# Optimization experiments

Measured on AMD Instinct MI355X. Metric: run time of the kernel, lower is better.

Reference implementation:

```python
import jax, jax.numpy as jnp
import numpy as np


def setup_inputs() -> dict:
    key = jax.random.key(0)
    k1, k2, k3 = jax.random.split(key, 3)
    B, C, H, W = 64, 2048, 14, 14
    M, NC = 32, 396
    x = jax.random.normal(k1, (B, C, H, W), dtype=jnp.float32)
    Wa = jax.random.normal(k2, (M, C), dtype=jnp.float32) * (1.0 / np.sqrt(C))
    ba = jnp.zeros((M,), dtype=jnp.float32)
    Wc = jax.random.normal(k3, (NC, M * C), dtype=jnp.float32) * (1.0 / np.sqrt(M * C))
    bc = jnp.zeros((NC,), dtype=jnp.float32)
    return {"x": x, "Wa": Wa, "ba": ba, "Wc": Wc, "bc": bc}


def reference(x, Wa, ba, Wc, bc):
    # x: [B, C, H, W]
    B, C, H, W = x.shape
    M = Wa.shape[0]
    # 1x1 conv == channel contraction; attention maps [B, M, H, W]
    A = jax.nn.sigmoid(jnp.einsum('bchw,mc->bmhw', x, Wa) + ba[None, :, None, None])
    # BAP: per-head attention-weighted global average pool -> [B, M, C]
    bap = jnp.einsum('bchw,bmhw->bmc', x, A) / (H * W)
    feats = bap.reshape(B, M * C)  # concat head-major, matching torch cat order
    return feats @ Wc.T + bc
```

## Files before the change

kernel.cpp:

```cpp
#include <hip/hip_runtime.h>
#include <hip/hip_bf16.h>
#include <cstdint>

#define B_N 64
#define C_N 2048
#define HW_N 196
#define HWP 224
#define M_N 32
#define NC_N 396
#define K_N 65536
#define CCH 256
#define NCH 8
#define KCH 64
#define ZSTRIDE (B_N * M_N * HW_N)

typedef __attribute__((ext_vector_type(8))) short bf16x8;
typedef __attribute__((ext_vector_type(4))) float f32x4;

__device__ inline short f2bf(float x) {
  union { float f; unsigned u; } v; v.f = x;
  unsigned r = (v.u + 0x7FFFu + ((v.u >> 16) & 1u)) >> 16;
  return (short)r;
}

__device__ inline unsigned packbf2(float lo, float hi) {
  return ((unsigned)(unsigned short)f2bf(hi) << 16) |
         (unsigned)(unsigned short)f2bf(lo);
}

__global__ __launch_bounds__(256) void k1a_partial(
    const float* __restrict__ x, const float* __restrict__ Wa,
    float* __restrict__ z) {
  __shared__ short waT[32][264];
  __shared__ short xT[2][208][40];
  const int t = threadIdx.x;
  const int w = t >> 6, lane = t & 63, lq = lane >> 4, ln = lane & 15;
  const int cx = blockIdx.x, b = blockIdx.y;
  const int c0 = cx * CCH;

  unsigned* xTw0 = (unsigned*)xT[0];
  unsigned* xTw1 = (unsigned*)xT[1];
  if (t < 240) { xTw0[196 * 20 + t] = 0u; xTw1[196 * 20 + t] = 0u; }
  for (int i = t; i < 2048; i += 256) {
    int m = i >> 6, f4 = i & 63;
    float4 v = *(const float4*)(Wa + (size_t)m * C_N + c0 + f4 * 4);
    uint2 pk;
    pk.x = packbf2(v.x, v.y);
    pk.y = packbf2(v.z, v.w);
    *(uint2*)((char*)waT + m * 528 + f4 * 8) = pk;
  }

  f32x4 acc[4][2];
#pragma unroll
  for (int ti = 0; ti < 4; ++ti) {
    acc[ti][0] = (f32x4){0.f, 0.f, 0.f, 0.f};
    acc[ti][1] = (f32x4){0.f, 0.f, 0.f, 0.f};
  }

  const float* __restrict__ xb0 = x + (size_t)b * (C_N * HW_N) + (size_t)c0 * HW_N;
  const int p0 = t & 15;
  const int q0 = t >> 4;

  float4 fa0, fb0, fa1, fb1, fa2, fb2, fa3, fb3;
  auto LD = [&](int ss) {
    const float* xs = xb0 + (size_t)ss * 32 * HW_N;
    const float* r0 = xs + (2 * p0) * HW_N + 4 * q0;
    fa0 = *(const float4*)r0;
    fb0 = *(const float4*)(r0 + HW_N);
    fa1 = *(const float4*)(r0 + 64);
    fb1 = *(const float4*)(r0 + 64 + HW_N);
    fa2 = *(const float4*)(r0 + 128);
    fb2 = *(const float4*)(r0 + 128 + HW_N);
    if (t < 16) {
      const float* r3 = xs + (2 * t) * HW_N + 192;
      fa3 = *(const float4*)r3;
      fb3 = *(const float4*)(r3 + HW_N);
    }
  };
  auto STORE = [&](unsigned* xw) {
    unsigned* d0 = xw + q0 * 80 + p0;
    d0[0]  = packbf2(fa0.x, fb0.x);
    d0[20] = packbf2(fa0.y, fb0.y);
    d0[40] = packbf2(fa0.z, fb0.z);
    d0[60] = packbf2(fa0.w, fb0.w);
    unsigned* d1 = d0 + 1280;
    d1[0]  = packbf2(fa1.x, fb1.x);
    d1[20] = packbf2(fa1.y, fb1.y);
    d1[40] = packbf2(fa1.z, fb1.z);
    d1[60] = packbf2(fa1.w, fb1.w);
    unsigned* d2 = d0 + 2560;
    d2[0]  = packbf2(fa2.x, fb2.x);
    d2[20] = packbf2(fa2.y, fb2.y);
    d2[40] = packbf2(fa2.z, fb2.z);
    d2[60] = packbf2(fa2.w, fb2.w);
    if (t < 16) {
      unsigned* d3 = xw + 48 * 80 + t;
      d3[0]  = packbf2(fa3.x, fb3.x);
      d3[20] = packbf2(fa3.y, fb3.y);
      d3[40] = packbf2(fa3.z, fb3.z);
      d3[60] = packbf2(fa3.w, fb3.w);
    }
  };

  LD(0);
  STORE(xTw0);
  __syncthreads();

  for (int ss = 0; ss < 8; ++ss) {
    if (ss < 7) LD(ss + 1);
    const char* xb = (const char*)xT[ss & 1];
    const int kb = ss * 64 + lq * 16;
    bf16x8 af0 = *(const bf16x8*)((const char*)waT + ln * 528 + kb);
    bf16x8 af1 = *(const bf16x8*)((const char*)waT + (16 + ln) * 528 + kb);
#pragma unroll
    for (int ti = 0; ti < 4; ++ti) {
      int ht = w + ti * 4;
      if (ht < 13) {
        bf16x8 bfr = *(const bf16x8*)(xb + (ht * 16 + ln) * 80 + lq * 16);
        acc[ti][0] = __builtin_amdgcn_mfma_f32_16x16x32_bf16(af0, bfr, acc[ti][0], 0, 0, 0);
        acc[ti][1] = __builtin_amdgcn_mfma_f32_16x16x32_bf16(af1, bfr, acc[ti][1], 0, 0, 0);
      }
    }
    if (ss < 7) STORE((ss & 1) ? xTw0 : xTw1);
    __syncthreads();
  }

  float* zc = z + (size_t)(cx * B_N + b) * (M_N * HW_N);
#pragma unroll
  for (int ti = 0; ti < 4; ++ti) {
    int ht = w + ti * 4;
    if (ht < 13) {
      int hw = ht * 16 + ln;
      if (hw < HW_N) {
#pragma unroll
        for (int mt = 0; mt < 2; ++mt) {
#pragma unroll
          for (int r = 0; r < 4; ++r) {
            int m = mt * 16 + lq * 4 + r;
            zc[(size_t)m * HW_N + hw] = acc[ti][mt][r];
          }
        }
      }
    }
  }
}

__global__ __launch_bounds__(256) void k1b_sig(
    const float* __restrict__ z, const float* __restrict__ ba,
    short* __restrict__ Apad) {
  int idx = blockIdx.x * 256 + threadIdx.x;
  int b = idx / (M_N * HWP);
  int r = idx - b * (M_N * HWP);
  int m = r / HWP;
  int hw = r - m * HWP;
  short out = 0;
  if (hw < HW_N) {
    float s = ba[m];
    size_t base = ((size_t)b * M_N + m) * HW_N + hw;
#pragma unroll
    for (int cx = 0; cx < NCH; ++cx)
      s += z[(size_t)cx * ZSTRIDE + base];
    out = f2bf(1.f / (1.f + __expf(-s)));
  }
  Apad[idx] = out;
}

__global__ __launch_bounds__(256) void k2_bap(
    const float* __restrict__ x, const short* __restrict__ Apad,
    short* __restrict__ featsb) {
  __shared__ short tb[8192];
  const int t = threadIdx.x;
  const int w = t >> 6, lane = t & 63, lq = lane >> 4, ln = lane & 15;
  const int cx = blockIdx.x;
  const int bq = blockIdx.y;
  const int cl = w * 16 + ln;
  const int c = cx * 64 + cl;
  const float sc = 1.f / (float)HW_N;
  const int och = cl >> 5, lq2w = (cl >> 3) & 3, j = cl & 7;

#pragma unroll
  for (int bi = 0; bi < 4; ++bi) {
    const int b = bq * 4 + bi;
    const float* __restrict__ xrow = x + (size_t)b * (C_N * HW_N) + (size_t)c * HW_N;
    const short* __restrict__ ap0 = Apad + ((size_t)b * M_N + ln) * HWP + lq * 8;
    const short* __restrict__ ap1 = ap0 + 16 * HWP;

    f32x4 d0 = {0.f, 0.f, 0.f, 0.f}, d1 = {0.f, 0.f, 0.f, 0.f};
#pragma unroll
    for (int s = 0; s < 7; ++s) {
      bf16x8 a0 = *(const bf16x8*)(ap0 + s * 32);
      bf16x8 a1 = *(const bf16x8*)(ap1 + s * 32);
      bf16x8 bfr;
      const int h = s * 32 + lq * 8;
      if (s < 6) {
        float4 b0 = *(const float4*)(xrow + h);
        float4 b1 = *(const float4*)(xrow + h + 4);
        bfr[0]=f2bf(b0.x); bfr[1]=f2bf(b0.y); bfr[2]=f2bf(b0.z); bfr[3]=f2bf(b0.w);
        bfr[4]=f2bf(b1.x); bfr[5]=f2bf(b1.y); bfr[6]=f2bf(b1.z); bfr[7]=f2bf(b1.w);
      } else {
        float4 b0 = make_float4(0.f, 0.f, 0.f, 0.f);
        if (lq == 0) b0 = *(const float4*)(xrow + h);
        bfr[0]=f2bf(b0.x); bfr[1]=f2bf(b0.y); bfr[2]=f2bf(b0.z); bfr[3]=f2bf(b0.w);
        bfr[4]=0; bfr[5]=0; bfr[6]=0; bfr[7]=0;
      }
      d0 = __builtin_amdgcn_mfma_f32_16x16x32_bf16(a0, bfr, d0, 0, 0, 0);
      d1 = __builtin_amdgcn_mfma_f32_16x16x32_bf16(a1, bfr, d1, 0, 0, 0);
    }
#pragma unroll
    for (int r = 0; r < 4; ++r) {
      int m0 = lq * 4 + r;
      tb[m0 * 256 + och * 128 + lq2w * 32 + bi * 8 + j]        = f2bf(d0[r] * sc);
      tb[(16 + m0) * 256 + och * 128 + lq2w * 32 + bi * 8 + j] = f2bf(d1[r] * sc);
    }
  }
  __syncthreads();

  const int me = t >> 3, oche = (t >> 2) & 1, lq2e = t & 3;
  const short* srcp = tb + t * 32;
  uint4 v0 = *(const uint4*)(srcp);
  uint4 v1 = *(const uint4*)(srcp + 8);
  uint4 v2 = *(const uint4*)(srcp + 16);
  uint4 v3 = *(const uint4*)(srcp + 24);
  const int sg = me * 64 + cx * 2 + oche;
  const int bt = bq >> 2;
  short* dst = featsb + (size_t)(sg * 4 + bt) * 512 + lq2e * 128 + (bq & 3) * 32;
  *(uint4*)(dst)      = v0;
  *(uint4*)(dst + 8)  = v1;
  *(uint4*)(dst + 16) = v2;
  *(uint4*)(dst + 24) = v3;
}

__global__ __launch_bounds__(256) void k3_cls(
    const short* __restrict__ featsb, const float* __restrict__ Wc,
    float* __restrict__ partial) {
  const int t = threadIdx.x;
  const int w = t >> 6, lane = t & 63, lq = lane >> 4, ln = lane & 15;
  const int n = blockIdx.x * 64 + w * 16 + ln;
  const int nc = n < NC_N ? n : NC_N - 1;
  const int kc = blockIdx.y;
  const size_t k0 = (size_t)kc * 1024;
  const float* __restrict__ wrow = Wc + (size_t)nc * K_N + k0 + lq * 8;
  const short* __restrict__ fb = featsb + (size_t)(kc * 32) * 2048 + lane * 8;

  f32x4 acc0 = {0.f,0.f,0.f,0.f}, acc1 = {0.f,0.f,0.f,0.f};
  f32x4 acc2 = {0.f,0.f,0.f,0.f}, acc3 = {0.f,0.f,0.f,0.f};

  float4 cw0 = *(const float4*)(wrow);
  float4 cw1 = *(const float4*)(wrow + 4);
  bf16x8 ca0 = *(const bf16x8*)(fb);
  bf16x8 ca1 = *(const bf16x8*)(fb + 512);
  bf16x8 ca2 = *(const bf16x8*)(fb + 1024);
  bf16x8 ca3 = *(const bf16x8*)(fb + 1536);

#pragma unroll
  for (int s = 0; s < 32; ++s) {
    float4 nw0, nw1; bf16x8 na0, na1, na2, na3;
    if (s < 31) {
      const float* wn = wrow + (s + 1) * 32;
      nw0 = *(const float4*)(wn);
      nw1 = *(const float4*)(wn + 4);
      const short* fs = fb + (size_t)(s + 1) * 2048;
      na0 = *(const bf16x8*)(fs);
      na1 = *(const bf16x8*)(fs + 512);
      na2 = *(const bf16x8*)(fs + 1024);
      na3 = *(const bf16x8*)(fs + 1536);
    }
    bf16x8 bfr;
    bfr[0]=f2bf(cw0.x); bfr[1]=f2bf(cw0.y); bfr[2]=f2bf(cw0.z); bfr[3]=f2bf(cw0.w);
    bfr[4]=f2bf(cw1.x); bfr[5]=f2bf(cw1.y); bfr[6]=f2bf(cw1.z); bfr[7]=f2bf(cw1.w);
    acc0 = __builtin_amdgcn_mfma_f32_16x16x32_bf16(ca0, bfr, acc0, 0, 0, 0);
    acc1 = __builtin_amdgcn_mfma_f32_16x16x32_bf16(ca1, bfr, acc1, 0, 0, 0);
    acc2 = __builtin_amdgcn_mfma_f32_16x16x32_bf16(ca2, bfr, acc2, 0, 0, 0);
    acc3 = __builtin_amdgcn_mfma_f32_16x16x32_bf16(ca3, bfr, acc3, 0, 0, 0);
    if (s < 31) {
      cw0 = nw0; cw1 = nw1;
      ca0 = na0; ca1 = na1; ca2 = na2; ca3 = na3;
    }
  }
  if (n < NC_N) {
    float* po = partial + (size_t)kc * (B_N * NC_N) + n;
#pragma unroll
    for (int r = 0; r < 4; ++r) {
      int br = lq * 4 + r;
      po[(size_t)br * NC_N]        = acc0[r];
      po[(size_t)(16 + br) * NC_N] = acc1[r];
      po[(size_t)(32 + br) * NC_N] = acc2[r];
      po[(size_t)(48 + br) * NC_N] = acc3[r];
    }
  }
}

__global__ __launch_bounds__(256) void k4_reduce(
    const float* __restrict__ partial, const float* __restrict__ bc,
    float* __restrict__ out) {
  int idx = blockIdx.x * 256 + threadIdx.x;
  if (idx >= B_N * NC_N) return;
  int n = idx % NC_N;
  float s = bc[n];
#pragma unroll 8
  for (int kc = 0; kc < KCH; ++kc) s += partial[(size_t)kc * (B_N * NC_N) + idx];
  out[idx] = s;
}

extern "C" void kernel_launch(void* const* d_in, const int* in_sizes, int n_in,
                              void* d_out, int out_size, void* d_ws, size_t ws_size,
                              hipStream_t stream) {
  const float* x  = (const float*)d_in[0];
  const float* Wa = (const float*)d_in[1];
  const float* ba = (const float*)d_in[2];
  const float* Wc = (const float*)d_in[3];
  const float* bc = (const float*)d_in[4];
  float* out = (float*)d_out;

  char* wsb = (char*)d_ws;
  short* Apad    = (short*)(wsb);
  short* featsb  = (short*)(wsb + (1u  << 20));
  float* partial = (float*)(wsb + (10u << 20));
  float* zbuf    = (float*)(wsb + (10u << 20));
  (void)ws_size; (void)in_sizes; (void)n_in; (void)out_size;

  hipLaunchKernelGGL(k1a_partial, dim3(NCH, B_N), dim3(256), 0, stream,
                     x, Wa, zbuf);
  hipLaunchKernelGGL(k1b_sig, dim3(1792), dim3(256), 0, stream,
                     zbuf, ba, Apad);
  hipLaunchKernelGGL(k2_bap, dim3(32, 16), dim3(256), 0, stream,
                     x, Apad, featsb);
  hipLaunchKernelGGL(k3_cls, dim3(7, KCH), dim3(256), 0, stream,
                     featsb, Wc, partial);
  hipLaunchKernelGGL(k4_reduce, dim3(99), dim3(256), 0, stream,
                     partial, bc, out);
}
```

Before: 270.5 us.

## Halve channel/K chunks, batch-interleave BAP loads, triple-buffer classifier prefetch

Halves the per-block channel chunk in the attention-logit kernel, which doubles the grid, and halves the K chunk in the classifier, which doubles the split-K partials. Padding rows of the x tile are now masked in registers instead of zero-filled in shared memory. The BAP kernel interleaves its four batches inside each step and prefetches the next step's x loads across all of them. The classifier moves to a three-slot register prefetch pipeline. More blocks and deeper prefetch aim to raise occupancy and hide memory latency, at the cost of more partial-sum traffic, a longer reduction, and more register pressure.

```diff
diff --git a/kernel.cpp b/kernel.cpp
--- a/kernel.cpp
+++ b/kernel.cpp
@@ -9,9 +9,9 @@
 #define M_N 32
 #define NC_N 396
 #define K_N 65536
-#define CCH 256
-#define NCH 8
-#define KCH 64
+#define CCH 128
+#define NCH 16
+#define KCH 128
 #define ZSTRIDE (B_N * M_N * HW_N)
 
 typedef __attribute__((ext_vector_type(8))) short bf16x8;
@@ -31,8 +31,8 @@
 __global__ __launch_bounds__(256) void k1a_partial(
     const float* __restrict__ x, const float* __restrict__ Wa,
     float* __restrict__ z) {
-  __shared__ short waT[32][264];
-  __shared__ short xT[2][208][40];
+  __shared__ short waT[32][136];
+  __shared__ short xT[2][196][40];
   const int t = threadIdx.x;
   const int w = t >> 6, lane = t & 63, lq = lane >> 4, ln = lane & 15;
   const int cx = blockIdx.x, b = blockIdx.y;
@@ -40,14 +40,13 @@
 
   unsigned* xTw0 = (unsigned*)xT[0];
   unsigned* xTw1 = (unsigned*)xT[1];
-  if (t < 240) { xTw0[196 * 20 + t] = 0u; xTw1[196 * 20 + t] = 0u; }
-  for (int i = t; i < 2048; i += 256) {
-    int m = i >> 6, f4 = i & 63;
+  for (int i = t; i < 1024; i += 256) {
+    int m = i >> 5, f4 = i & 31;
     float4 v = *(const float4*)(Wa + (size_t)m * C_N + c0 + f4 * 4);
     uint2 pk;
     pk.x = packbf2(v.x, v.y);
     pk.y = packbf2(v.z, v.w);
-    *(uint2*)((char*)waT + m * 528 + f4 * 8) = pk;
+    *(uint2*)((char*)waT + m * 272 + f4 * 8) = pk;
   }
 
   f32x4 acc[4][2];
@@ -106,22 +105,26 @@
   STORE(xTw0);
   __syncthreads();
 
-  for (int ss = 0; ss < 8; ++ss) {
-    if (ss < 7) LD(ss + 1);
+  const bf16x8 bzero = {0, 0, 0, 0, 0, 0, 0, 0};
+  for (int ss = 0; ss < 4; ++ss) {
+    if (ss < 3) LD(ss + 1);
     const char* xb = (const char*)xT[ss & 1];
     const int kb = ss * 64 + lq * 16;
-    bf16x8 af0 = *(const bf16x8*)((const char*)waT + ln * 528 + kb);
-    bf16x8 af1 = *(const bf16x8*)((const char*)waT + (16 + ln) * 528 + kb);
+    bf16x8 af0 = *(const bf16x8*)((const char*)waT + ln * 272 + kb);
+    bf16x8 af1 = *(const bf16x8*)((const char*)waT + (16 + ln) * 272 + kb);
 #pragma unroll
     for (int ti = 0; ti < 4; ++ti) {
       int ht = w + ti * 4;
       if (ht < 13) {
-        bf16x8 bfr = *(const bf16x8*)(xb + (ht * 16 + ln) * 80 + lq * 16);
+        int hwrow = ht * 16 + ln;
+        int rr = hwrow < HW_N ? hwrow : 0;
+        bf16x8 v = *(const bf16x8*)(xb + rr * 80 + lq * 16);
+        bf16x8 bfr = (hwrow < HW_N) ? v : bzero;
         acc[ti][0] = __builtin_amdgcn_mfma_f32_16x16x32_bf16(af0, bfr, acc[ti][0], 0, 0, 0);
         acc[ti][1] = __builtin_amdgcn_mfma_f32_16x16x32_bf16(af1, bfr, acc[ti][1], 0, 0, 0);
       }
     }
-    if (ss < 7) STORE((ss & 1) ? xTw0 : xTw1);
+    if (ss < 3) STORE((ss & 1) ? xTw0 : xTw1);
     __syncthreads();
   }
 
@@ -177,40 +180,73 @@
   const int c = cx * 64 + cl;
   const float sc = 1.f / (float)HW_N;
   const int och = cl >> 5, lq2w = (cl >> 3) & 3, j = cl & 7;
-
+  const size_t bstr = (size_t)C_N * HW_N;
+  const float* __restrict__ xrow0 = x + (size_t)(bq * 4) * bstr + (size_t)c * HW_N;
+
+  const short* apb[4];
+#pragma unroll
+  for (int bi = 0; bi < 4; ++bi)
+    apb[bi] = Apad + ((size_t)(bq * 4 + bi) * M_N + ln) * HWP + lq * 8;
+
+  f32x4 d0[4], d1[4];
 #pragma unroll
   for (int bi = 0; bi < 4; ++bi) {
-    const int b = bq * 4 + bi;
-    const float* __restrict__ xrow = x + (size_t)b * (C_N * HW_N) + (size_t)c * HW_N;
-    const short* __restrict__ ap0 = Apad + ((size_t)b * M_N + ln) * HWP + lq * 8;
-    const short* __restrict__ ap1 = ap0 + 16 * HWP;
-
-    f32x4 d0 = {0.f, 0.f, 0.f, 0.f}, d1 = {0.f, 0.f, 0.f, 0.f};
-#pragma unroll
-    for (int s = 0; s < 7; ++s) {
-      bf16x8 a0 = *(const bf16x8*)(ap0 + s * 32);
-      bf16x8 a1 = *(const bf16x8*)(ap1 + s * 32);
+    d0[bi] = (f32x4){0.f, 0.f, 0.f, 0.f};
+    d1[bi] = (f32x4){0.f, 0.f, 0.f, 0.f};
+  }
+
+  float4 xa[4], xc[4];
+#pragma unroll
+  for (int bi = 0; bi < 4; ++bi) {
+    const float* p = xrow0 + bi * bstr + lq * 8;
+    xa[bi] = *(const float4*)p;
+    xc[bi] = *(const float4*)(p + 4);
+  }
+
+#pragma unroll
+  for (int s = 0; s < 7; ++s) {
+    float4 na[4], nc[4];
+    if (s < 6) {
+      if (s + 1 < 6) {
+        const int h = (s + 1) * 32 + lq * 8;
+#pragma unroll
+        for (int bi = 0; bi < 4; ++bi) {
+          const float* p = xrow0 + bi * bstr + h;
+          na[bi] = *(const float4*)p;
+          nc[bi] = *(const float4*)(p + 4);
+        }
+      } else {
+#pragma unroll
+        for (int bi = 0; bi < 4; ++bi) {
+          float4 z4 = make_float4(0.f, 0.f, 0.f, 0.f);
+          na[bi] = z4; nc[bi] = z4;
+          if (lq == 0) na[bi] = *(const float4*)(xrow0 + bi * bstr + 192);
+        }
+      }
+    }
+#pragma unroll
+    for (int bi = 0; bi < 4; ++bi) {
+      bf16x8 a0 = *(const bf16x8*)(apb[bi] + s * 32);
+      bf16x8 a1 = *(const bf16x8*)(apb[bi] + 16 * HWP + s * 32);
       bf16x8 bfr;
-      const int h = s * 32 + lq * 8;
-      if (s < 6) {
-        float4 b0 = *(const float4*)(xrow + h);
-        float4 b1 = *(const float4*)(xrow + h + 4);
-        bfr[0]=f2bf(b0.x); bfr[1]=f2bf(b0.y); bfr[2]=f2bf(b0.z); bfr[3]=f2bf(b0.w);
-        bfr[4]=f2bf(b1.x); bfr[5]=f2bf(b1.y); bfr[6]=f2bf(b1.z); bfr[7]=f2bf(b1.w);
-      } else {
-        float4 b0 = make_float4(0.f, 0.f, 0.f, 0.f);
-        if (lq == 0) b0 = *(const float4*)(xrow + h);
-        bfr[0]=f2bf(b0.x); bfr[1]=f2bf(b0.y); bfr[2]=f2bf(b0.z); bfr[3]=f2bf(b0.w);
-        bfr[4]=0; bfr[5]=0; bfr[6]=0; bfr[7]=0;
-      }
-      d0 = __builtin_amdgcn_mfma_f32_16x16x32_bf16(a0, bfr, d0, 0, 0, 0);
-      d1 = __builtin_amdgcn_mfma_f32_16x16x32_bf16(a1, bfr, d1, 0, 0, 0);
-    }
+      bfr[0]=f2bf(xa[bi].x); bfr[1]=f2bf(xa[bi].y); bfr[2]=f2bf(xa[bi].z); bfr[3]=f2bf(xa[bi].w);
+      bfr[4]=f2bf(xc[bi].x); bfr[5]=f2bf(xc[bi].y); bfr[6]=f2bf(xc[bi].z); bfr[7]=f2bf(xc[bi].w);
+      d0[bi] = __builtin_amdgcn_mfma_f32_16x16x32_bf16(a0, bfr, d0[bi], 0, 0, 0);
+      d1[bi] = __builtin_amdgcn_mfma_f32_16x16x32_bf16(a1, bfr, d1[bi], 0, 0, 0);
+    }
+    if (s < 6) {
+#pragma unroll
+      for (int bi = 0; bi < 4; ++bi) { xa[bi] = na[bi]; xc[bi] = nc[bi]; }
+    }
+  }
+
+#pragma unroll
+  for (int bi = 0; bi < 4; ++bi) {
 #pragma unroll
     for (int r = 0; r < 4; ++r) {
       int m0 = lq * 4 + r;
-      tb[m0 * 256 + och * 128 + lq2w * 32 + bi * 8 + j]        = f2bf(d0[r] * sc);
-      tb[(16 + m0) * 256 + och * 128 + lq2w * 32 + bi * 8 + j] = f2bf(d1[r] * sc);
+      tb[m0 * 256 + och * 128 + lq2w * 32 + bi * 8 + j]        = f2bf(d0[bi][r] * sc);
+      tb[(16 + m0) * 256 + och * 128 + lq2w * 32 + bi * 8 + j] = f2bf(d1[bi][r] * sc);
     }
   }
   __syncthreads();
@@ -238,45 +274,41 @@
   const int n = blockIdx.x * 64 + w * 16 + ln;
   const int nc = n < NC_N ? n : NC_N - 1;
   const int kc = blockIdx.y;
-  const size_t k0 = (size_t)kc * 1024;
-  const float* __restrict__ wrow = Wc + (size_t)nc * K_N + k0 + lq * 8;
-  const short* __restrict__ fb = featsb + (size_t)(kc * 32) * 2048 + lane * 8;
+  const float* __restrict__ wrow = Wc + (size_t)nc * K_N + (size_t)kc * 512 + lq * 8;
+  const short* __restrict__ fb = featsb + (size_t)(kc * 16) * 2048 + lane * 8;
 
   f32x4 acc0 = {0.f,0.f,0.f,0.f}, acc1 = {0.f,0.f,0.f,0.f};
   f32x4 acc2 = {0.f,0.f,0.f,0.f}, acc3 = {0.f,0.f,0.f,0.f};
 
-  float4 cw0 = *(const float4*)(wrow);
-  float4 cw1 = *(const float4*)(wrow + 4);
-  bf16x8 ca0 = *(const bf16x8*)(fb);
-  bf16x8 ca1 = *(const bf16x8*)(fb + 512);
-  bf16x8 ca2 = *(const bf16x8*)(fb + 1024);
-  bf16x8 ca3 = *(const bf16x8*)(fb + 1536);
-
-#pragma unroll
-  for (int s = 0; s < 32; ++s) {
-    float4 nw0, nw1; bf16x8 na0, na1, na2, na3;
-    if (s < 31) {
-      const float* wn = wrow + (s + 1) * 32;
-      nw0 = *(const float4*)(wn);
-      nw1 = *(const float4*)(wn + 4);
-      const short* fs = fb + (size_t)(s + 1) * 2048;
-      na0 = *(const bf16x8*)(fs);
-      na1 = *(const bf16x8*)(fs + 512);
-      na2 = *(const bf16x8*)(fs + 1024);
-      na3 = *(const bf16x8*)(fs + 1536);
-    }
+  float4 pw0[3], pw1[3];
+  bf16x8 pa0[3], pa1[3], pa2[3], pa3[3];
+#define K3LD(S, SL) do {                                           \
+    const float* wn_ = wrow + (S) * 32;                            \
+    pw0[SL] = *(const float4*)wn_;                                 \
+    pw1[SL] = *(const float4*)(wn_ + 4);                           \
+    const short* fs_ = fb + (size_t)(S) * 2048;                    \
+    pa0[SL] = *(const bf16x8*)(fs_);                               \
+    pa1[SL] = *(const bf16x8*)(fs_ + 512);                         \
+    pa2[SL] = *(const bf16x8*)(fs_ + 1024);                        \
+    pa3[SL] = *(const bf16x8*)(fs_ + 1536);                        \
+  } while (0)
+
+  K3LD(0, 0);
+  K3LD(1, 1);
+#pragma unroll
+  for (int s = 0; s < 16; ++s) {
+    if (s + 2 < 16) K3LD(s + 2, (s + 2) % 3);
+    const int sl = s % 3;
     bf16x8 bfr;
-    bfr[0]=f2bf(cw0.x); bfr[1]=f2bf(cw0.y); bfr[2]=f2bf(cw0.z); bfr[3]=f2bf(cw0.w);
-    bfr[4]=f2bf(cw1.x); bfr[5]=f2bf(cw1.y); bfr[6]=f2bf(cw1.z); bfr[7]=f2bf(cw1.w);
-    acc0 = __builtin_amdgcn_mfma_f32_16x16x32_bf16(ca0, bfr, acc0, 0, 0, 0);
-    acc1 = __builtin_amdgcn_mfma_f32_16x16x32_bf16(ca1, bfr, acc1, 0, 0, 0);
-    acc2 = __builtin_amdgcn_mfma_f32_16x16x32_bf16(ca2, bfr, acc2, 0, 0, 0);
-    acc3 = __builtin_amdgcn_mfma_f32_16x16x32_bf16(ca3, bfr, acc3, 0, 0, 0);
-    if (s < 31) {
-      cw0 = nw0; cw1 = nw1;
-      ca0 = na0; ca1 = na1; ca2 = na2; ca3 = na3;
-    }
-  }
+    bfr[0]=f2bf(pw0[sl].x); bfr[1]=f2bf(pw0[sl].y); bfr[2]=f2bf(pw0[sl].z); bfr[3]=f2bf(pw0[sl].w);
+    bfr[4]=f2bf(pw1[sl].x); bfr[5]=f2bf(pw1[sl].y); bfr[6]=f2bf(pw1[sl].z); bfr[7]=f2bf(pw1[sl].w);
+    acc0 = __builtin_amdgcn_mfma_f32_16x16x32_bf16(pa0[sl], bfr, acc0, 0, 0, 0);
+    acc1 = __builtin_amdgcn_mfma_f32_16x16x32_bf16(pa1[sl], bfr, acc1, 0, 0, 0);
+    acc2 = __builtin_amdgcn_mfma_f32_16x16x32_bf16(pa2[sl], bfr, acc2, 0, 0, 0);
+    acc3 = __builtin_amdgcn_mfma_f32_16x16x32_bf16(pa3[sl], bfr, acc3, 0, 0, 0);
+  }
+#undef K3LD
+
   if (n < NC_N) {
     float* po = partial + (size_t)kc * (B_N * NC_N) + n;
 #pragma unroll
@@ -315,8 +347,8 @@
   char* wsb = (char*)d_ws;
   short* Apad    = (short*)(wsb);
   short* featsb  = (short*)(wsb + (1u  << 20));
-  float* partial = (float*)(wsb + (10u << 20));
   float* zbuf    = (float*)(wsb + (10u << 20));
+  float* partial = (float*)(wsb + (40u << 20));
   (void)ws_size; (void)in_sizes; (void)n_in; (void)out_size;
 
   hipLaunchKernelGGL(k1a_partial, dim3(NCH, B_N), dim3(256), 0, stream,
```

New measurement: 282.9 us. 4.6% more time.

## Prefetch x rows across batch pairs in BAP and double k3 split-K chunks

Applied to the files above, without the earlier changes.

The BAP kernel now handles two batches per step with four live accumulator sets, and software-prefetches the next x row segment before the MFMAs run. This is meant to hide global-load latency. The classifier kernel's split-K count goes from 64 to 128 chunks of half the size to launch more blocks and raise parallelism. That doubles the partial-sum buffer and the reduction work, so the partial buffer is moved to a new workspace offset.

```diff
diff --git a/kernel.cpp b/kernel.cpp
--- a/kernel.cpp
+++ b/kernel.cpp
@@ -11,7 +11,7 @@
 #define K_N 65536
 #define CCH 256
 #define NCH 8
-#define KCH 64
+#define KCH 128
 #define ZSTRIDE (B_N * M_N * HW_N)
 
 typedef __attribute__((ext_vector_type(8))) short bf16x8;
@@ -177,40 +177,78 @@
   const int c = cx * 64 + cl;
   const float sc = 1.f / (float)HW_N;
   const int och = cl >> 5, lq2w = (cl >> 3) & 3, j = cl & 7;
-
+  const size_t bstr = (size_t)C_N * HW_N;
+  const float* __restrict__ xrow0 = x + (size_t)(bq * 4) * bstr + (size_t)c * HW_N;
+
+  f32x4 d0[4], d1[4];
 #pragma unroll
   for (int bi = 0; bi < 4; ++bi) {
-    const int b = bq * 4 + bi;
-    const float* __restrict__ xrow = x + (size_t)b * (C_N * HW_N) + (size_t)c * HW_N;
-    const short* __restrict__ ap0 = Apad + ((size_t)b * M_N + ln) * HWP + lq * 8;
-    const short* __restrict__ ap1 = ap0 + 16 * HWP;
-
-    f32x4 d0 = {0.f, 0.f, 0.f, 0.f}, d1 = {0.f, 0.f, 0.f, 0.f};
+    d0[bi] = (f32x4){0.f, 0.f, 0.f, 0.f};
+    d1[bi] = (f32x4){0.f, 0.f, 0.f, 0.f};
+  }
+
+#pragma unroll
+  for (int bp = 0; bp < 2; ++bp) {
+    const float* __restrict__ xrA = xrow0 + (size_t)(bp * 2) * bstr;
+    const float* __restrict__ xrB = xrA + bstr;
+    const short* __restrict__ apA = Apad + ((size_t)(bq * 4 + bp * 2) * M_N + ln) * HWP + lq * 8;
+    const short* __restrict__ apB = apA + (size_t)M_N * HWP;
+
+    float4 xaA = *(const float4*)(xrA + lq * 8);
+    float4 xcA = *(const float4*)(xrA + lq * 8 + 4);
+    float4 xaB = *(const float4*)(xrB + lq * 8);
+    float4 xcB = *(const float4*)(xrB + lq * 8 + 4);
+
 #pragma unroll
     for (int s = 0; s < 7; ++s) {
-      bf16x8 a0 = *(const bf16x8*)(ap0 + s * 32);
-      bf16x8 a1 = *(const bf16x8*)(ap1 + s * 32);
-      bf16x8 bfr;
-      const int h = s * 32 + lq * 8;
+      float4 naA, ncA, naB, ncB;
       if (s < 6) {
-        float4 b0 = *(const float4*)(xrow + h);
-        float4 b1 = *(const float4*)(xrow + h + 4);
-        bfr[0]=f2bf(b0.x); bfr[1]=f2bf(b0.y); bfr[2]=f2bf(b0.z); bfr[3]=f2bf(b0.w);
-        bfr[4]=f2bf(b1.x); bfr[5]=f2bf(b1.y); bfr[6]=f2bf(b1.z); bfr[7]=f2bf(b1.w);
-      } else {
-        float4 b0 = make_float4(0.f, 0.f, 0.f, 0.f);
-        if (lq == 0) b0 = *(const float4*)(xrow + h);
-        bfr[0]=f2bf(b0.x); bfr[1]=f2bf(b0.y); bfr[2]=f2bf(b0.z); bfr[3]=f2bf(b0.w);
-        bfr[4]=0; bfr[5]=0; bfr[6]=0; bfr[7]=0;
-      }
-      d0 = __builtin_amdgcn_mfma_f32_16x16x32_bf16(a0, bfr, d0, 0, 0, 0);
-      d1 = __builtin_amdgcn_mfma_f32_16x16x32_bf16(a1, bfr, d1, 0, 0, 0);
-    }
+        if (s + 1 < 6) {
+          const int h = (s + 1) * 32 + lq * 8;
+          naA = *(const float4*)(xrA + h);
+          ncA = *(const float4*)(xrA + h + 4);
+          naB = *(const float4*)(xrB + h);
+          ncB = *(const float4*)(xrB + h + 4);
+        } else {
+          float4 z4 = make_float4(0.f, 0.f, 0.f, 0.f);
+          naA = z4; ncA = z4; naB = z4; ncB = z4;
+          if (lq == 0) {
+            naA = *(const float4*)(xrA + 192);
+            naB = *(const float4*)(xrB + 192);
+          }
+        }
+      }
+      {
+        bf16x8 a0 = *(const bf16x8*)(apA + s * 32);
+        bf16x8 a1 = *(const bf16x8*)(apA + 16 * HWP + s * 32);
+        bf16x8 bfr;
+        bfr[0]=f2bf(xaA.x); bfr[1]=f2bf(xaA.y); bfr[2]=f2bf(xaA.z); bfr[3]=f2bf(xaA.w);
+        bfr[4]=f2bf(xcA.x); bfr[5]=f2bf(xcA.y); bfr[6]=f2bf(xcA.z); bfr[7]=f2bf(xcA.w);
+        d0[bp*2] = __builtin_amdgcn_mfma_f32_16x16x32_bf16(a0, bfr, d0[bp*2], 0, 0, 0);
+        d1[bp*2] = __builtin_amdgcn_mfma_f32_16x16x32_bf16(a1, bfr, d1[bp*2], 0, 0, 0);
+      }
+      {
+        bf16x8 a0 = *(const bf16x8*)(apB + s * 32);
+        bf16x8 a1 = *(const bf16x8*)(apB + 16 * HWP + s * 32);
+        bf16x8 bfr;
+        bfr[0]=f2bf(xaB.x); bfr[1]=f2bf(xaB.y); bfr[2]=f2bf(xaB.z); bfr[3]=f2bf(xaB.w);
+        bfr[4]=f2bf(xcB.x); bfr[5]=f2bf(xcB.y); bfr[6]=f2bf(xcB.z); bfr[7]=f2bf(xcB.w);
+        d0[bp*2+1] = __builtin_amdgcn_mfma_f32_16x16x32_bf16(a0, bfr, d0[bp*2+1], 0, 0, 0);
+        d1[bp*2+1] = __builtin_amdgcn_mfma_f32_16x16x32_bf16(a1, bfr, d1[bp*2+1], 0, 0, 0);
+      }
+      if (s < 6) {
+        xaA = naA; xcA = ncA; xaB = naB; xcB = ncB;
+      }
+    }
+  }
+
+#pragma unroll
+  for (int bi = 0; bi < 4; ++bi) {
 #pragma unroll
     for (int r = 0; r < 4; ++r) {
       int m0 = lq * 4 + r;
-      tb[m0 * 256 + och * 128 + lq2w * 32 + bi * 8 + j]        = f2bf(d0[r] * sc);
-      tb[(16 + m0) * 256 + och * 128 + lq2w * 32 + bi * 8 + j] = f2bf(d1[r] * sc);
+      tb[m0 * 256 + och * 128 + lq2w * 32 + bi * 8 + j]        = f2bf(d0[bi][r] * sc);
+      tb[(16 + m0) * 256 + och * 128 + lq2w * 32 + bi * 8 + j] = f2bf(d1[bi][r] * sc);
     }
   }
   __syncthreads();
@@ -238,9 +276,9 @@
   const int n = blockIdx.x * 64 + w * 16 + ln;
   const int nc = n < NC_N ? n : NC_N - 1;
   const int kc = blockIdx.y;
-  const size_t k0 = (size_t)kc * 1024;
+  const size_t k0 = (size_t)kc * 512;
   const float* __restrict__ wrow = Wc + (size_t)nc * K_N + k0 + lq * 8;
-  const short* __restrict__ fb = featsb + (size_t)(kc * 32) * 2048 + lane * 8;
+  const short* __restrict__ fb = featsb + (size_t)(kc * 16) * 2048 + lane * 8;
 
   f32x4 acc0 = {0.f,0.f,0.f,0.f}, acc1 = {0.f,0.f,0.f,0.f};
   f32x4 acc2 = {0.f,0.f,0.f,0.f}, acc3 = {0.f,0.f,0.f,0.f};
@@ -253,9 +291,9 @@
   bf16x8 ca3 = *(const bf16x8*)(fb + 1536);
 
 #pragma unroll
-  for (int s = 0; s < 32; ++s) {
+  for (int s = 0; s < 16; ++s) {
     float4 nw0, nw1; bf16x8 na0, na1, na2, na3;
-    if (s < 31) {
+    if (s < 15) {
       const float* wn = wrow + (s + 1) * 32;
       nw0 = *(const float4*)(wn);
       nw1 = *(const float4*)(wn + 4);
@@ -272,7 +310,7 @@
     acc1 = __builtin_amdgcn_mfma_f32_16x16x32_bf16(ca1, bfr, acc1, 0, 0, 0);
     acc2 = __builtin_amdgcn_mfma_f32_16x16x32_bf16(ca2, bfr, acc2, 0, 0, 0);
     acc3 = __builtin_amdgcn_mfma_f32_16x16x32_bf16(ca3, bfr, acc3, 0, 0, 0);
-    if (s < 31) {
+    if (s < 15) {
       cw0 = nw0; cw1 = nw1;
       ca0 = na0; ca1 = na1; ca2 = na2; ca3 = na3;
     }
@@ -315,8 +353,8 @@
   char* wsb = (char*)d_ws;
   short* Apad    = (short*)(wsb);
   short* featsb  = (short*)(wsb + (1u  << 20));
-  float* partial = (float*)(wsb + (10u << 20));
   float* zbuf    = (float*)(wsb + (10u << 20));
+  float* partial = (float*)(wsb + (40u << 20));
   (void)ws_size; (void)in_sizes; (void)n_in; (void)out_size;
 
   hipLaunchKernelGGL(k1a_partial, dim3(NCH, B_N), dim3(256), 0, stream,
```

After: 280.1 us. +3.6%, slower.

## Split classifier K into more chunks and halve batches per BAP block

Applied to the files above, without the earlier changes.

The classifier GEMM now splits K into 256 chunks instead of 64, with each block handling 256 K elements. The explicit register double-buffering is dropped, and launch bounds ask for higher occupancy. The BAP kernel processes 2 batches per block over twice as many blocks, with a smaller shared tile and a matching featsb layout. The partial buffer moves to its own workspace region so it no longer aliases zbuf. This raises parallelism in the split-K and BAP stages, but it makes the final reduction read 4x more partial data and adds more atomic-free partial writes.

```diff
diff --git a/kernel.cpp b/kernel.cpp
--- a/kernel.cpp
+++ b/kernel.cpp
@@ -11,7 +11,7 @@
 #define K_N 65536
 #define CCH 256
 #define NCH 8
-#define KCH 64
+#define KCH 256
 #define ZSTRIDE (B_N * M_N * HW_N)
 
 typedef __attribute__((ext_vector_type(8))) short bf16x8;
@@ -168,20 +168,21 @@
 __global__ __launch_bounds__(256) void k2_bap(
     const float* __restrict__ x, const short* __restrict__ Apad,
     short* __restrict__ featsb) {
-  __shared__ short tb[8192];
+  __shared__ short tb[4096];
   const int t = threadIdx.x;
   const int w = t >> 6, lane = t & 63, lq = lane >> 4, ln = lane & 15;
   const int cx = blockIdx.x;
-  const int bq = blockIdx.y;
+  const int bq2 = blockIdx.y;
   const int cl = w * 16 + ln;
   const int c = cx * 64 + cl;
   const float sc = 1.f / (float)HW_N;
   const int och = cl >> 5, lq2w = (cl >> 3) & 3, j = cl & 7;
-
-#pragma unroll
-  for (int bi = 0; bi < 4; ++bi) {
-    const int b = bq * 4 + bi;
-    const float* __restrict__ xrow = x + (size_t)b * (C_N * HW_N) + (size_t)c * HW_N;
+  const size_t bstr = (size_t)C_N * HW_N;
+
+#pragma unroll
+  for (int bi = 0; bi < 2; ++bi) {
+    const int b = bq2 * 2 + bi;
+    const float* __restrict__ xrow = x + (size_t)b * bstr + (size_t)c * HW_N;
     const short* __restrict__ ap0 = Apad + ((size_t)b * M_N + ln) * HWP + lq * 8;
     const short* __restrict__ ap1 = ap0 + 16 * HWP;
 
@@ -209,28 +210,24 @@
 #pragma unroll
     for (int r = 0; r < 4; ++r) {
       int m0 = lq * 4 + r;
-      tb[m0 * 256 + och * 128 + lq2w * 32 + bi * 8 + j]        = f2bf(d0[r] * sc);
-      tb[(16 + m0) * 256 + och * 128 + lq2w * 32 + bi * 8 + j] = f2bf(d1[r] * sc);
+      tb[((m0 * 2 + och) * 4 + lq2w) * 16 + bi * 8 + j]        = f2bf(d0[r] * sc);
+      tb[(((16 + m0) * 2 + och) * 4 + lq2w) * 16 + bi * 8 + j] = f2bf(d1[r] * sc);
     }
   }
   __syncthreads();
 
   const int me = t >> 3, oche = (t >> 2) & 1, lq2e = t & 3;
-  const short* srcp = tb + t * 32;
+  const short* srcp = tb + t * 16;
   uint4 v0 = *(const uint4*)(srcp);
   uint4 v1 = *(const uint4*)(srcp + 8);
-  uint4 v2 = *(const uint4*)(srcp + 16);
-  uint4 v3 = *(const uint4*)(srcp + 24);
   const int sg = me * 64 + cx * 2 + oche;
-  const int bt = bq >> 2;
-  short* dst = featsb + (size_t)(sg * 4 + bt) * 512 + lq2e * 128 + (bq & 3) * 32;
-  *(uint4*)(dst)      = v0;
-  *(uint4*)(dst + 8)  = v1;
-  *(uint4*)(dst + 16) = v2;
-  *(uint4*)(dst + 24) = v3;
-}
-
-__global__ __launch_bounds__(256) void k3_cls(
+  const int bt = bq2 >> 3;
+  short* dst = featsb + (size_t)(sg * 4 + bt) * 512 + lq2e * 128 + (bq2 & 7) * 16;
+  *(uint4*)(dst)     = v0;
+  *(uint4*)(dst + 8) = v1;
+}
+
+__global__ __launch_bounds__(256, 8) void k3_cls(
     const short* __restrict__ featsb, const float* __restrict__ Wc,
     float* __restrict__ partial) {
   const int t = threadIdx.x;
@@ -238,45 +235,31 @@
   const int n = blockIdx.x * 64 + w * 16 + ln;
   const int nc = n < NC_N ? n : NC_N - 1;
   const int kc = blockIdx.y;
-  const size_t k0 = (size_t)kc * 1024;
-  const float* __restrict__ wrow = Wc + (size_t)nc * K_N + k0 + lq * 8;
-  const short* __restrict__ fb = featsb + (size_t)(kc * 32) * 2048 + lane * 8;
+  const float* __restrict__ wrow = Wc + (size_t)nc * K_N + (size_t)kc * 256 + lq * 8;
+  const short* __restrict__ fb = featsb + (size_t)(kc * 8) * 2048 + lane * 8;
 
   f32x4 acc0 = {0.f,0.f,0.f,0.f}, acc1 = {0.f,0.f,0.f,0.f};
   f32x4 acc2 = {0.f,0.f,0.f,0.f}, acc3 = {0.f,0.f,0.f,0.f};
 
-  float4 cw0 = *(const float4*)(wrow);
-  float4 cw1 = *(const float4*)(wrow + 4);
-  bf16x8 ca0 = *(const bf16x8*)(fb);
-  bf16x8 ca1 = *(const bf16x8*)(fb + 512);
-  bf16x8 ca2 = *(const bf16x8*)(fb + 1024);
-  bf16x8 ca3 = *(const bf16x8*)(fb + 1536);
-
-#pragma unroll
-  for (int s = 0; s < 32; ++s) {
-    float4 nw0, nw1; bf16x8 na0, na1, na2, na3;
-    if (s < 31) {
-      const float* wn = wrow + (s + 1) * 32;
-      nw0 = *(const float4*)(wn);
-      nw1 = *(const float4*)(wn + 4);
-      const short* fs = fb + (size_t)(s + 1) * 2048;
-      na0 = *(const bf16x8*)(fs);
-      na1 = *(const bf16x8*)(fs + 512);
-      na2 = *(const bf16x8*)(fs + 1024);
-      na3 = *(const bf16x8*)(fs + 1536);
-    }
+#pragma unroll
+  for (int s = 0; s < 8; ++s) {
+    const float* wn = wrow + s * 32;
+    float4 cw0 = *(const float4*)(wn);
+    float4 cw1 = *(const float4*)(wn + 4);
+    const short* fs = fb + (size_t)s * 2048;
+    bf16x8 a0 = *(const bf16x8*)(fs);
+    bf16x8 a1 = *(const bf16x8*)(fs + 512);
+    bf16x8 a2 = *(const bf16x8*)(fs + 1024);
+    bf16x8 a3 = *(const bf16x8*)(fs + 1536);
     bf16x8 bfr;
     bfr[0]=f2bf(cw0.x); bfr[1]=f2bf(cw0.y); bfr[2]=f2bf(cw0.z); bfr[3]=f2bf(cw0.w);
     bfr[4]=f2bf(cw1.x); bfr[5]=f2bf(cw1.y); bfr[6]=f2bf(cw1.z); bfr[7]=f2bf(cw1.w);
-    acc0 = __builtin_amdgcn_mfma_f32_16x16x32_bf16(ca0, bfr, acc0, 0, 0, 0);
-    acc1 = __builtin_amdgcn_mfma_f32_16x16x32_bf16(ca1, bfr, acc1, 0, 0, 0);
-    acc2 = __builtin_amdgcn_mfma_f32_16x16x32_bf16(ca2, bfr, acc2, 0, 0, 0);
-    acc3 = __builtin_amdgcn_mfma_f32_16x16x32_bf16(ca3, bfr, acc3, 0, 0, 0);
-    if (s < 31) {
-      cw0 = nw0; cw1 = nw1;
-      ca0 = na0; ca1 = na1; ca2 = na2; ca3 = na3;
-    }
-  }
+    acc0 = __builtin_amdgcn_mfma_f32_16x16x32_bf16(a0, bfr, acc0, 0, 0, 0);
+    acc1 = __builtin_amdgcn_mfma_f32_16x16x32_bf16(a1, bfr, acc1, 0, 0, 0);
+    acc2 = __builtin_amdgcn_mfma_f32_16x16x32_bf16(a2, bfr, acc2, 0, 0, 0);
+    acc3 = __builtin_amdgcn_mfma_f32_16x16x32_bf16(a3, bfr, acc3, 0, 0, 0);
+  }
+
   if (n < NC_N) {
     float* po = partial + (size_t)kc * (B_N * NC_N) + n;
 #pragma unroll
@@ -297,7 +280,7 @@
   if (idx >= B_N * NC_N) return;
   int n = idx % NC_N;
   float s = bc[n];
-#pragma unroll 8
+#pragma unroll 32
   for (int kc = 0; kc < KCH; ++kc) s += partial[(size_t)kc * (B_N * NC_N) + idx];
   out[idx] = s;
 }
@@ -315,15 +298,15 @@
   char* wsb = (char*)d_ws;
   short* Apad    = (short*)(wsb);
   short* featsb  = (short*)(wsb + (1u  << 20));
-  float* partial = (float*)(wsb + (10u << 20));
   float* zbuf    = (float*)(wsb + (10u << 20));
+  float* partial = (float*)(wsb + (23u << 20));
   (void)ws_size; (void)in_sizes; (void)n_in; (void)out_size;
 
   hipLaunchKernelGGL(k1a_partial, dim3(NCH, B_N), dim3(256), 0, stream,
                      x, Wa, zbuf);
   hipLaunchKernelGGL(k1b_sig, dim3(1792), dim3(256), 0, stream,
                      zbuf, ba, Apad);
-  hipLaunchKernelGGL(k2_bap, dim3(32, 16), dim3(256), 0, stream,
+  hipLaunchKernelGGL(k2_bap, dim3(32, 32), dim3(256), 0, stream,
                      x, Apad, featsb);
   hipLaunchKernelGGL(k3_cls, dim3(7, KCH), dim3(256), 0, stream,
                      featsb, Wc, partial);
```

After: 277.2 us. 1.02x slower.
